# Kernel tuning notes

Hardware: AMD Instinct MI355X
Metric: run time of the kernel (lower is better)

Reference implementation:

```python
import jax, jax.numpy as jnp
import numpy as np

B, N, K, E = 2, 131072, 20, 256  # batch, points, n_slot, feat/embed dim
GN_GROUPS = 4
IOU_THR = 0.5
SCORE_THR = 0.04
TEMP = 0.05


def setup_inputs() -> dict:
    key = jax.random.key(0)
    ks = jax.random.split(key, 6)
    wscale = 1.0 / np.sqrt(E)
    return {
        "features": jax.random.normal(ks[0], (B, N, E), jnp.float32),
        "slots": jax.random.normal(ks[1], (B, K, E), jnp.float32),
        "w1": jax.random.normal(ks[2], (E, E), jnp.float32) * wscale,
        "b1": jax.random.normal(ks[3], (E,), jnp.float32) * 0.01,
        "gn_g": jnp.ones((E,), jnp.float32),
        "gn_b": jnp.zeros((E,), jnp.float32),
        "w2": jax.random.normal(ks[4], (E, E), jnp.float32) * wscale,
        "b2": jax.random.normal(ks[5], (E,), jnp.float32) * 0.01,
    }


def _l2norm(x, axis):
    n = jnp.linalg.norm(x, axis=axis, keepdims=True)
    return x / jnp.maximum(n, 1e-12)  # F.normalize semantics


def _nms_filter(mask):
    # mask: [N, K] soft instance probabilities (rows sum to 1)
    scores = mask.mean(axis=0)                       # [K]
    valid = scores >= SCORE_THR
    order = jnp.argsort(-scores)                     # descending score
    sm = mask[:, order]                              # [N, K] sorted columns
    bm = (sm > 0.5).astype(mask.dtype).T             # [K, N] binary masks
    areas = bm.sum(axis=1)                           # [K]
    inter = bm @ bm.T                                # [K, K] pairwise intersections
    union = areas[:, None] + areas[None, :] - inter
    iou = inter / (union + 1e-8)
    idx = jnp.arange(K)
    sup0 = ~valid[order]                             # invalid slots pre-suppressed

    def body(i, sup):
        keep_i = ~sup[i]
        return sup | (keep_i & (iou[i] > IOU_THR) & (idx > i))

    sup = jax.lax.fori_loop(0, K, body, sup0)
    kept = ~sup                                      # [K]
    # kept columns are packed (in score order) into the left of the output;
    # dropped columns are routed to a dump column K which is sliced away.
    pos = jnp.cumsum(kept) - 1
    cols = jnp.where(kept, pos, K)
    out = jnp.zeros((mask.shape[0], K + 1), mask.dtype).at[:, cols].set(sm)
    out = out[:, :K]
    # per-point renormalization over kept masks (zeros stay zero if none kept)
    return out / (out.sum(axis=1, keepdims=True) + 1e-8)


def reference(features, slots, w1, b1, gn_g, gn_b, w2, b2):
    # object_mlp: Conv1d(1x1) -> GroupNorm(4) -> ReLU -> Conv1d(1x1)
    x = jnp.einsum('bke,oe->bok', slots, w1) + b1[None, :, None]   # [B, E, K]
    xg = x.reshape(B, GN_GROUPS, E // GN_GROUPS, K)
    mu = xg.mean(axis=(2, 3), keepdims=True)
    var = xg.var(axis=(2, 3), keepdims=True)
    xg = (xg - mu) * jax.lax.rsqrt(var + 1e-5)
    x = xg.reshape(B, E, K) * gn_g[None, :, None] + gn_b[None, :, None]
    x = jax.nn.relu(x)
    slot = jnp.einsum('bek,fe->bfk', x, w2) + b2[None, :, None]    # [B, F=E, K]

    fn = _l2norm(features, axis=-1)                                # [B, N, E]
    sn = _l2norm(slot, axis=1)                                     # [B, E, K]
    logits = jnp.einsum('bnd,bdk->bnk', fn, sn) / TEMP
    mask = jax.nn.softmax(logits, axis=-1)                         # [B, N, K]

    out = jax.vmap(_nms_filter)(mask)                              # [B, N, K]
    return out.transpose(0, 2, 1)                                  # [B, K, N]
```

## Files before the change

### kernel.cpp

```cpp
#include <hip/hip_runtime.h>

#define B_ 2
#define N_ 131072
#define K_ 20
#define E_ 256
#define TEMP_ 0.05f
#define SCORE_THR_ 0.04f

#define WS_SCORE 0
#define WS_XN    1024
#define WS_SN    16384
#define WS_MASK  32768
#define WS_SPART 6291456

__device__ inline float wave_sum(float v) {
    #pragma unroll
    for (int off = 32; off; off >>= 1) v += __shfl_xor(v, off, 64);
    return v;
}

__global__ __launch_bounds__(256) void kA1(const float* __restrict__ slots,
                                           const float* __restrict__ w1,
                                           const float* __restrict__ b1,
                                           const float* __restrict__ gn_g,
                                           const float* __restrict__ gn_b,
                                           float* __restrict__ ws) {
    __shared__ __align__(16) float slds[20 * 260];
    __shared__ float red[2];
    const int t = threadIdx.x;
    const int b = blockIdx.x >> 2, g = blockIdx.x & 3;
    if (t < 2) red[t] = 0.f;
    const float* sb = slots + (size_t)b * K_ * E_;
    #pragma unroll
    for (int i = 0; i < 20; ++i) slds[i * 260 + t] = sb[i * 256 + t];
    __syncthreads();

    const int c = t >> 2, q = t & 3;
    const int o = g * 64 + c;
    const float* w1r = w1 + (size_t)o * E_;
    float acc[5] = {0.f, 0.f, 0.f, 0.f, 0.f};
    for (int e4 = 0; e4 < 64; ++e4) {
        const float4 w4 = *(const float4*)(w1r + e4 * 4);
        #pragma unroll
        for (int kk = 0; kk < 5; ++kk) {
            const float4 s4 = *(const float4*)&slds[(q * 5 + kk) * 260 + e4 * 4];
            acc[kk] += w4.x * s4.x + w4.y * s4.y + w4.z * s4.z + w4.w * s4.w;
        }
    }
    const float bias = b1[o];
    float s1 = 0.f, s2 = 0.f;
    #pragma unroll
    for (int kk = 0; kk < 5; ++kk) {
        acc[kk] += bias;
        s1 += acc[kk];
        s2 += acc[kk] * acc[kk];
    }
    s1 = wave_sum(s1);
    s2 = wave_sum(s2);
    if ((t & 63) == 0) { atomicAdd(&red[0], s1); atomicAdd(&red[1], s2); }
    __syncthreads();
    const float mean = red[0] * (1.f / 1280.f);
    const float var  = red[1] * (1.f / 1280.f) - mean * mean;
    const float rstd = rsqrtf(var + 1e-5f);
    const float gg = gn_g[o], gb = gn_b[o];
    float* xn = ws + WS_XN + (size_t)b * K_ * E_;
    #pragma unroll
    for (int kk = 0; kk < 5; ++kk) {
        float v = (acc[kk] - mean) * rstd * gg + gb;
        v = v > 0.f ? v : 0.f;
        xn[(q * 5 + kk) * 256 + o] = v;
    }
}

__global__ __launch_bounds__(256) void kA2(const float* __restrict__ w2,
                                           const float* __restrict__ b2,
                                           float* __restrict__ ws) {
    __shared__ __align__(16) float xv[256];
    __shared__ float wred[4];
    const int t = threadIdx.x;
    const int b = blockIdx.x / 20, k = blockIdx.x % 20;
    const float* xn = ws + WS_XN + (size_t)(b * 20 + k) * 256;
    xv[t] = xn[t];
    __syncthreads();
    const float* w2r = w2 + (size_t)t * 256;
    float acc = 0.f;
    for (int e4 = 0; e4 < 64; ++e4) {
        const float4 w4 = *(const float4*)(w2r + e4 * 4);
        const float4 x4 = *(const float4*)&xv[e4 * 4];
        acc += w4.x * x4.x + w4.y * x4.y + w4.z * x4.z + w4.w * x4.w;
    }
    acc += b2[t];
    float sq = wave_sum(acc * acc);
    if ((t & 63) == 0) wred[t >> 6] = sq;
    __syncthreads();
    const float nsq = wred[0] + wred[1] + wred[2] + wred[3];
    const float inv = 1.f / fmaxf(sqrtf(nsq), 1e-12f);
    ws[WS_SN + (size_t)(b * 20 + k) * 256 + t] = acc * inv;
}

__global__ __launch_bounds__(256, 2) void kB(const float* __restrict__ feat,
                                             float* __restrict__ ws) {
    __shared__ __align__(16) float snl[20 * 260];
    __shared__ __align__(16) float fl[32 * 260];
    __shared__ float pl[640];
    __shared__ float wsum[4][20];
    const int t = threadIdx.x;
    const int b = blockIdx.x >> 9;
    const int n0 = (blockIdx.x & 511) << 8;
    const float* sng = ws + WS_SN + (size_t)b * 5120;
    #pragma unroll
    for (int i = 0; i < 20; ++i) snl[i * 260 + t] = sng[i * 256 + t];
    const int p = t >> 3, s = t & 7;
    const int lane = t & 63, w = t >> 6;
    float sreg0 = 0.f, sreg1 = 0.f, sreg2 = 0.f;
    const float4* gbase = (const float4*)(feat + ((size_t)b * N_ + n0) * E_);
    float* mgbase = ws + WS_MASK + (size_t)b * 20 * N_ + n0;
    __syncthreads();

    for (int c = 0; c < 8; ++c) {
        const float4* g4 = gbase + (size_t)c * 2048;
        #pragma unroll
        for (int i = 0; i < 8; ++i) {
            const int idx = t + (i << 8);
            const float4 v = g4[idx];
            const int pp = idx >> 6, cc = idx & 63;
            *(float4*)&fl[pp * 260 + (cc << 2)] = v;
        }
        __syncthreads();
        float acc[20];
        float nr = 0.f;
        #pragma unroll
        for (int k = 0; k < 20; ++k) acc[k] = 0.f;
        const float* frow = &fl[p * 260];
        #pragma unroll
        for (int j = 0; j < 8; ++j) {
            const int col = (s << 2) + (j << 5);
            const float4 f4 = *(const float4*)&frow[col];
            nr += f4.x * f4.x + f4.y * f4.y + f4.z * f4.z + f4.w * f4.w;
            #pragma unroll
            for (int k = 0; k < 20; ++k) {
                const float4 s4 = *(const float4*)&snl[k * 260 + col];
                acc[k] += f4.x * s4.x + f4.y * s4.y + f4.z * s4.z + f4.w * s4.w;
            }
        }
        #pragma unroll
        for (int off = 1; off < 8; off <<= 1) {
            nr += __shfl_xor(nr, off, 64);
            #pragma unroll
            for (int k = 0; k < 20; ++k) acc[k] += __shfl_xor(acc[k], off, 64);
        }
        const float scl = rsqrtf(fmaxf(nr, 1e-24f)) * (1.f / TEMP_);
        float m = -1e30f;
        #pragma unroll
        for (int k = 0; k < 20; ++k) { acc[k] *= scl; m = fmaxf(m, acc[k]); }
        float su = 0.f;
        #pragma unroll
        for (int k = 0; k < 20; ++k) { acc[k] = __expf(acc[k] - m); su += acc[k]; }
        const float r = 1.f / su;
        float v0 = 0.f, v1 = 0.f, v2 = 0.f;
        #pragma unroll
        for (int k = 0; k < 8; ++k) {
            if (s == k) {
                v0 = acc[k] * r;
                v1 = acc[k + 8] * r;
                v2 = (k < 4) ? acc[k + 16] * r : 0.f;
            }
        }
        pl[(s << 5) + p] = v0;
        pl[((s + 8) << 5) + p] = v1;
        if (s < 4) pl[((s + 16) << 5) + p] = v2;
        sreg0 += v0; sreg1 += v1; sreg2 += v2;
        __syncthreads();
        #pragma unroll
        for (int i = 0; i < 3; ++i) {
            const int idx = t + (i << 8);
            if (idx < 640) {
                const int k = idx >> 5, pp = idx & 31;
                mgbase[(size_t)k * N_ + (c << 5) + pp] = pl[idx];
            }
        }
        __syncthreads();
    }
    #pragma unroll
    for (int off = 8; off < 64; off <<= 1) {
        sreg0 += __shfl_xor(sreg0, off, 64);
        sreg1 += __shfl_xor(sreg1, off, 64);
        sreg2 += __shfl_xor(sreg2, off, 64);
    }
    if (lane < 8) {
        wsum[w][lane] = sreg0;
        wsum[w][lane + 8] = sreg1;
        if (lane < 4) wsum[w][lane + 16] = sreg2;
    }
    __syncthreads();
    if (t < 20) {
        const float sum = wsum[0][t] + wsum[1][t] + wsum[2][t] + wsum[3][t];
        ws[WS_SPART + (size_t)blockIdx.x * 20 + t] = sum;
    }
}

__global__ __launch_bounds__(64) void kC(float* __restrict__ ws) {
    const int l = threadIdx.x;
    const int b = blockIdx.x / 20, k = blockIdx.x % 20;
    const float* sp = ws + WS_SPART;
    float sum = 0.f;
    #pragma unroll
    for (int i = 0; i < 8; ++i)
        sum += sp[(size_t)(b * 512 + l + i * 64) * 20 + k];
    sum = wave_sum(sum);
    if (l == 0) ws[WS_SCORE + blockIdx.x] = sum * (1.f / (float)N_);
}

__global__ __launch_bounds__(256) void kD(const float* __restrict__ ws,
                                          float* __restrict__ out) {
    __shared__ float sc[20];
    __shared__ int rnk[20];
    __shared__ int src[20];
    __shared__ int nk_s;
    const int t = threadIdx.x;
    const int b = blockIdx.x >> 9;
    const int n = (blockIdx.x & 511) * 256 + t;
    if (t < 20) sc[t] = ws[WS_SCORE + b * 20 + t];
    if (t == 0) nk_s = 0;
    __syncthreads();
    if (t < 20) {
        const float mys = sc[t];
        int rank = 0;
        for (int j = 0; j < 20; ++j) {
            const float o = sc[j];
            rank += (o > mys) || (o == mys && j < t);
        }
        rnk[t] = rank;
    }
    __syncthreads();
    if (t < 20 && sc[t] >= SCORE_THR_) {
        int pos = 0;
        for (int j = 0; j < 20; ++j)
            pos += (sc[j] >= SCORE_THR_) && (rnk[j] < rnk[t]);
        src[pos] = t;
        atomicAdd(&nk_s, 1);
    }
    __syncthreads();
    const int nk = nk_s;
    const float* mg = ws + WS_MASK + (size_t)b * 20 * N_;
    float mv[20];
    float den = 1e-8f;
    #pragma unroll
    for (int p = 0; p < 20; ++p) {
        float v = 0.f;
        if (p < nk) v = mg[(size_t)src[p] * N_ + n];
        mv[p] = v;
        den += v;
    }
    const float r = 1.f / den;
    float* og = out + (size_t)b * 20 * N_ + n;
    #pragma unroll
    for (int p = 0; p < 20; ++p) og[(size_t)p * N_] = (p < nk) ? mv[p] * r : 0.f;
}

extern "C" void kernel_launch(void* const* d_in, const int* in_sizes, int n_in,
                              void* d_out, int out_size, void* d_ws, size_t ws_size,
                              hipStream_t stream) {
    const float* feat  = (const float*)d_in[0];
    const float* slots = (const float*)d_in[1];
    const float* w1    = (const float*)d_in[2];
    const float* b1    = (const float*)d_in[3];
    const float* gng   = (const float*)d_in[4];
    const float* gnb   = (const float*)d_in[5];
    const float* w2    = (const float*)d_in[6];
    const float* b2    = (const float*)d_in[7];
    float* ws  = (float*)d_ws;
    float* out = (float*)d_out;

    kA1<<<8,    256, 0, stream>>>(slots, w1, b1, gng, gnb, ws);
    kA2<<<40,   256, 0, stream>>>(w2, b2, ws);
    kB <<<1024, 256, 0, stream>>>(feat, ws);
    kC <<<40,   64,  0, stream>>>(ws);
    kD <<<1024, 256, 0, stream>>>(ws, out);
}
```

Measured before the change: 431.9 us.

## Restructure kB to one point per thread, read slots via global/cache, vectorize kD

kB now assigns one point per thread and stages features in four 64-column chunks, with each thread reading its own LDS row. The normalized slot vectors are read straight from global memory instead of an LDS copy. This removes the 8-lane shuffle reductions and the LDS transpose for mask stores, since each thread writes its 20 mask values coalesced, and it reduces score partials with wave sums. kD processes four points per thread with float4 loads and stores and uses a quarter of the blocks. The risks are more register pressure and uniform global slot loads, which rely on the scalar or L1 cache.

```diff
diff --git a/kernel.cpp b/kernel.cpp
--- a/kernel.cpp
+++ b/kernel.cpp
@@ -99,103 +99,74 @@
 }
 
 __global__ __launch_bounds__(256, 2) void kB(const float* __restrict__ feat,
-                                             float* __restrict__ ws) {
-    __shared__ __align__(16) float snl[20 * 260];
-    __shared__ __align__(16) float fl[32 * 260];
-    __shared__ float pl[640];
+                                             const float* __restrict__ snb,
+                                             float* __restrict__ mask,
+                                             float* __restrict__ spart) {
+    __shared__ __align__(16) float fl[256 * 68];
     __shared__ float wsum[4][20];
     const int t = threadIdx.x;
     const int b = blockIdx.x >> 9;
     const int n0 = (blockIdx.x & 511) << 8;
-    const float* sng = ws + WS_SN + (size_t)b * 5120;
-    #pragma unroll
-    for (int i = 0; i < 20; ++i) snl[i * 260 + t] = sng[i * 256 + t];
-    const int p = t >> 3, s = t & 7;
-    const int lane = t & 63, w = t >> 6;
-    float sreg0 = 0.f, sreg1 = 0.f, sreg2 = 0.f;
-    const float4* gbase = (const float4*)(feat + ((size_t)b * N_ + n0) * E_);
-    float* mgbase = ws + WS_MASK + (size_t)b * 20 * N_ + n0;
-    __syncthreads();
-
-    for (int c = 0; c < 8; ++c) {
-        const float4* g4 = gbase + (size_t)c * 2048;
+
+    const float4* g4 = (const float4*)(feat + ((size_t)b * N_ + n0) * E_);
+    const float* snB = snb + (size_t)b * 5120;
+
+    float acc[20];
+    #pragma unroll
+    for (int k = 0; k < 20; ++k) acc[k] = 0.f;
+    float nr = 0.f;
+
+    #pragma unroll
+    for (int h = 0; h < 4; ++h) {
         #pragma unroll
-        for (int i = 0; i < 8; ++i) {
-            const int idx = t + (i << 8);
-            const float4 v = g4[idx];
-            const int pp = idx >> 6, cc = idx & 63;
-            *(float4*)&fl[pp * 260 + (cc << 2)] = v;
+        for (int i = 0; i < 16; ++i) {
+            const int f = (i << 8) + t;
+            const int p = f >> 4, e4 = f & 15;
+            const float4 v = g4[(size_t)p * 64 + (h << 4) + e4];
+            *(float4*)&fl[p * 68 + (e4 << 2)] = v;
         }
         __syncthreads();
-        float acc[20];
-        float nr = 0.f;
-        #pragma unroll
-        for (int k = 0; k < 20; ++k) acc[k] = 0.f;
-        const float* frow = &fl[p * 260];
-        #pragma unroll
-        for (int j = 0; j < 8; ++j) {
-            const int col = (s << 2) + (j << 5);
-            const float4 f4 = *(const float4*)&frow[col];
+        const float* frow = &fl[t * 68];
+        for (int e4 = 0; e4 < 16; ++e4) {
+            const float4 f4 = *(const float4*)&frow[e4 << 2];
             nr += f4.x * f4.x + f4.y * f4.y + f4.z * f4.z + f4.w * f4.w;
+            const float* sp = snB + (h << 6) + (e4 << 2);
             #pragma unroll
             for (int k = 0; k < 20; ++k) {
-                const float4 s4 = *(const float4*)&snl[k * 260 + col];
+                const float4 s4 = *(const float4*)&sp[k << 8];
                 acc[k] += f4.x * s4.x + f4.y * s4.y + f4.z * s4.z + f4.w * s4.w;
             }
         }
+        __syncthreads();
+    }
+
+    const float scl = rsqrtf(fmaxf(nr, 1e-24f)) * (1.f / TEMP_);
+    float m = -1e30f;
+    #pragma unroll
+    for (int k = 0; k < 20; ++k) { acc[k] *= scl; m = fmaxf(m, acc[k]); }
+    float su = 0.f;
+    #pragma unroll
+    for (int k = 0; k < 20; ++k) { acc[k] = __expf(acc[k] - m); su += acc[k]; }
+    const float r = 1.f / su;
+
+    float* mg = mask + (size_t)b * 20 * N_ + n0 + t;
+    #pragma unroll
+    for (int k = 0; k < 20; ++k) {
+        const float v = acc[k] * r;
+        mg[(size_t)k * N_] = v;
+        acc[k] = wave_sum(v);
+    }
+    const int lane = t & 63, w = t >> 6;
+    if (lane < 20) {
+        float v = 0.f;
         #pragma unroll
-        for (int off = 1; off < 8; off <<= 1) {
-            nr += __shfl_xor(nr, off, 64);
-            #pragma unroll
-            for (int k = 0; k < 20; ++k) acc[k] += __shfl_xor(acc[k], off, 64);
-        }
-        const float scl = rsqrtf(fmaxf(nr, 1e-24f)) * (1.f / TEMP_);
-        float m = -1e30f;
-        #pragma unroll
-        for (int k = 0; k < 20; ++k) { acc[k] *= scl; m = fmaxf(m, acc[k]); }
-        float su = 0.f;
-        #pragma unroll
-        for (int k = 0; k < 20; ++k) { acc[k] = __expf(acc[k] - m); su += acc[k]; }
-        const float r = 1.f / su;
-        float v0 = 0.f, v1 = 0.f, v2 = 0.f;
-        #pragma unroll
-        for (int k = 0; k < 8; ++k) {
-            if (s == k) {
-                v0 = acc[k] * r;
-                v1 = acc[k + 8] * r;
-                v2 = (k < 4) ? acc[k + 16] * r : 0.f;
-            }
-        }
-        pl[(s << 5) + p] = v0;
-        pl[((s + 8) << 5) + p] = v1;
-        if (s < 4) pl[((s + 16) << 5) + p] = v2;
-        sreg0 += v0; sreg1 += v1; sreg2 += v2;
-        __syncthreads();
-        #pragma unroll
-        for (int i = 0; i < 3; ++i) {
-            const int idx = t + (i << 8);
-            if (idx < 640) {
-                const int k = idx >> 5, pp = idx & 31;
-                mgbase[(size_t)k * N_ + (c << 5) + pp] = pl[idx];
-            }
-        }
-        __syncthreads();
-    }
-    #pragma unroll
-    for (int off = 8; off < 64; off <<= 1) {
-        sreg0 += __shfl_xor(sreg0, off, 64);
-        sreg1 += __shfl_xor(sreg1, off, 64);
-        sreg2 += __shfl_xor(sreg2, off, 64);
-    }
-    if (lane < 8) {
-        wsum[w][lane] = sreg0;
-        wsum[w][lane + 8] = sreg1;
-        if (lane < 4) wsum[w][lane + 16] = sreg2;
+        for (int k = 0; k < 20; ++k) if (lane == k) v = acc[k];
+        wsum[w][lane] = v;
     }
     __syncthreads();
     if (t < 20) {
         const float sum = wsum[0][t] + wsum[1][t] + wsum[2][t] + wsum[3][t];
-        ws[WS_SPART + (size_t)blockIdx.x * 20 + t] = sum;
+        spart[(size_t)blockIdx.x * 20 + t] = sum;
     }
 }
 
@@ -218,8 +189,8 @@
     __shared__ int src[20];
     __shared__ int nk_s;
     const int t = threadIdx.x;
-    const int b = blockIdx.x >> 9;
-    const int n = (blockIdx.x & 511) * 256 + t;
+    const int b = blockIdx.x >> 7;
+    const int n = ((blockIdx.x & 127) << 10) + (t << 2);
     if (t < 20) sc[t] = ws[WS_SCORE + b * 20 + t];
     if (t == 0) nk_s = 0;
     __syncthreads();
@@ -243,19 +214,26 @@
     __syncthreads();
     const int nk = nk_s;
     const float* mg = ws + WS_MASK + (size_t)b * 20 * N_;
-    float mv[20];
-    float den = 1e-8f;
+    float4 mv[20];
+    float4 den = {1e-8f, 1e-8f, 1e-8f, 1e-8f};
     #pragma unroll
     for (int p = 0; p < 20; ++p) {
-        float v = 0.f;
-        if (p < nk) v = mg[(size_t)src[p] * N_ + n];
+        float4 v = {0.f, 0.f, 0.f, 0.f};
+        if (p < nk) v = *(const float4*)&mg[(size_t)src[p] * N_ + n];
         mv[p] = v;
-        den += v;
-    }
-    const float r = 1.f / den;
+        den.x += v.x; den.y += v.y; den.z += v.z; den.w += v.w;
+    }
+    const float4 r = {1.f / den.x, 1.f / den.y, 1.f / den.z, 1.f / den.w};
     float* og = out + (size_t)b * 20 * N_ + n;
     #pragma unroll
-    for (int p = 0; p < 20; ++p) og[(size_t)p * N_] = (p < nk) ? mv[p] * r : 0.f;
+    for (int p = 0; p < 20; ++p) {
+        float4 o4 = {0.f, 0.f, 0.f, 0.f};
+        if (p < nk) {
+            o4.x = mv[p].x * r.x; o4.y = mv[p].y * r.y;
+            o4.z = mv[p].z * r.z; o4.w = mv[p].w * r.w;
+        }
+        *(float4*)&og[(size_t)p * N_] = o4;
+    }
 }
 
 extern "C" void kernel_launch(void* const* d_in, const int* in_sizes, int n_in,
@@ -274,7 +252,7 @@
 
     kA1<<<8,    256, 0, stream>>>(slots, w1, b1, gng, gnb, ws);
     kA2<<<40,   256, 0, stream>>>(w2, b2, ws);
-    kB <<<1024, 256, 0, stream>>>(feat, ws);
+    kB <<<1024, 256, 0, stream>>>(feat, ws + WS_SN, ws + WS_MASK, ws + WS_SPART);
     kC <<<40,   64,  0, stream>>>(ws);
-    kD <<<1024, 256, 0, stream>>>(ws, out);
-}
+    kD <<<256,  256, 0, stream>>>(ws, out);
+}
```

After: 443.3 us. 1.03x slower.
